# Optimization experiments

Measured on AMD Instinct MI355X. Metric: run time of the kernel, lower is better.

Reference implementation:

```python
import jax, jax.numpy as jnp
import numpy as np

NEG_INF = jnp.finfo(jnp.float32).min


def setup_inputs() -> dict:
    key = jax.random.key(0)
    ks = jax.random.split(key, 5)
    B, S, D = 2, 2048, 1024
    std = 0.02
    return {
        "x": jax.random.normal(ks[0], (B, S, D), dtype=jnp.float32),
        "attention_mask": jnp.ones((B, S), dtype=jnp.int32),
        "Wq": jax.random.normal(ks[1], (D, D), dtype=jnp.float32) * std,
        "Wk": jax.random.normal(ks[2], (D, D), dtype=jnp.float32) * std,
        "Wv": jax.random.normal(ks[3], (D, D), dtype=jnp.float32) * std,
        "Wo": jax.random.normal(ks[4], (D, D), dtype=jnp.float32) * std,
    }


def reference(x, attention_mask, Wq, Wk, Wv, Wo):
    B, S, D = x.shape
    H = 16
    Hd = D // H
    scale = jnp.float32(np.sqrt(Hd))

    # F.linear uses W @ x^T, i.e. x @ W.T
    def proj(x, W):
        return jnp.einsum('bsd,ed->bse', x, W).reshape(B, S, H, Hd).transpose(0, 2, 1, 3)

    q = proj(x, Wq)  # [B,H,S,Hd]
    k = proj(x, Wk)
    v = proj(x, Wv)

    scores = jnp.einsum('bhqd,bhkd->bhqk', q, k) / scale  # [B,H,S,S]
    causal = jnp.triu(jnp.ones((S, S), dtype=bool), k=1)
    scores = jnp.where(causal[None, None, :, :], NEG_INF, scores)
    key_pad = (attention_mask == 0)[:, None, None, :]  # [B,1,1,S]
    scores = jnp.where(key_pad, NEG_INF, scores)

    attn = jax.nn.softmax(scores, axis=-1)
    out = jnp.einsum('bhqk,bhkd->bhqd', attn, v)  # [B,H,S,Hd]
    out = out.transpose(0, 2, 1, 3).reshape(B, S, D)
    return jnp.einsum('bsd,ed->bse', out, Wo)
```

## Files before the change

### kernel.cpp

```cpp
#include <hip/hip_runtime.h>
#include <hip/hip_bf16.h>

typedef __attribute__((ext_vector_type(8))) short bf16x8;
typedef __attribute__((ext_vector_type(4))) short bf16x4;
typedef __attribute__((ext_vector_type(4))) float f32x4;

#define LOG2E 1.4426950408889634f
#define MBIAS 11.541560327111707f
#define NEGF  -3.0e38f

__device__ __forceinline__ void gl_lds16(const void* g, void* l) {
  __builtin_amdgcn_global_load_lds((const __attribute__((address_space(1))) void*)g,
                                   (__attribute__((address_space(3))) void*)l, 16, 0, 0);
}

__device__ __forceinline__ ushort f2bu(float x) {
  __hip_bfloat16 h = __float2bfloat16(x);
  return *(ushort*)&h;
}

__device__ __forceinline__ unsigned int fbits(float x) {
  union { float f; unsigned int u; } c; c.f = x; return c.u;
}

__global__ __launch_bounds__(256) void cast_bf16_k(const float* __restrict__ in,
                                                   ushort* __restrict__ out, int n4) {
  int i = blockIdx.x * 256 + threadIdx.x;
  if (i >= n4) return;
  float4 f = ((const float4*)in)[i];
  ushort4 u;
  u.x = f2bu(f.x); u.y = f2bu(f.y); u.z = f2bu(f.z); u.w = f2bu(f.w);
  ((ushort4*)out)[i] = u;
}

__global__ __launch_bounds__(256) void cast_w4_k(const float* __restrict__ a, const float* __restrict__ b,
                                                 const float* __restrict__ c, const float* __restrict__ d,
                                                 ushort* __restrict__ oa, ushort* __restrict__ ob,
                                                 ushort* __restrict__ oc, ushort* __restrict__ od) {
  int i = blockIdx.x * 256 + threadIdx.x;
  int wsel = i >> 18, j = i & 262143;
  const float* src = wsel == 0 ? a : wsel == 1 ? b : wsel == 2 ? c : d;
  ushort* dst      = wsel == 0 ? oa : wsel == 1 ? ob : wsel == 2 ? oc : od;
  float4 f = ((const float4*)src)[j];
  ushort4 u;
  u.x = f2bu(f.x); u.y = f2bu(f.y); u.z = f2bu(f.z); u.w = f2bu(f.w);
  ((ushort4*)dst)[j] = u;
}

template<int OUT_BF16>
__device__ __forceinline__ void gemm_body(const ushort* __restrict__ A, const ushort* __restrict__ B,
                                          void* __restrict__ C, int M, int N, int Kd, float scale,
                                          int bm, int bn, ushort (*As)[4096], ushort (*Bs)[4096]) {
  const int t  = threadIdx.x;
  const int l  = t & 63;
  const int w  = t >> 6;
  const int lr = l & 15, lg = l >> 4;
  const int wr = (w >> 1) * 64, wc = (w & 1) * 64;

  auto stage = [&](int buf, int ktE) {
    int idx = t, row = idx >> 2, ch = idx & 3;
    gl_lds16(A + (size_t)(bm + row) * Kd + ktE + ch * 8, &As[buf][idx * 8]);
    gl_lds16(B + (size_t)(bn + row) * Kd + ktE + ch * 8, &Bs[buf][idx * 8]);
    idx = t + 256; row = idx >> 2; ch = idx & 3;
    gl_lds16(A + (size_t)(bm + row) * Kd + ktE + ch * 8, &As[buf][idx * 8]);
    gl_lds16(B + (size_t)(bn + row) * Kd + ktE + ch * 8, &Bs[buf][idx * 8]);
  };

  f32x4 acc[4][4] = {};
  const int nK = Kd >> 5;

  stage(0, 0);
  stage(1, 32);
  int cur = 0;
  for (int k5 = 0; k5 < nK; ++k5) {
    if (k5 + 2 < nK) {
      int nb = cur + 2; if (nb >= 3) nb -= 3;
      stage(nb, (k5 + 2) << 5);
      asm volatile("s_waitcnt vmcnt(8)" ::: "memory");
    } else if (k5 + 1 < nK) {
      asm volatile("s_waitcnt vmcnt(4)" ::: "memory");
    } else {
      asm volatile("s_waitcnt vmcnt(0)" ::: "memory");
    }
    __builtin_amdgcn_s_barrier();

    bf16x8 af[4], bfr[4];
#pragma unroll
    for (int m = 0; m < 4; ++m)
      af[m] = *(const bf16x8*)&As[cur][(wr + m * 16 + lr) * 32 + lg * 8];
#pragma unroll
    for (int n = 0; n < 4; ++n)
      bfr[n] = *(const bf16x8*)&Bs[cur][(wc + n * 16 + lr) * 32 + lg * 8];
#pragma unroll
    for (int m = 0; m < 4; ++m)
#pragma unroll
      for (int n = 0; n < 4; ++n)
        acc[m][n] = __builtin_amdgcn_mfma_f32_16x16x32_bf16(af[m], bfr[n], acc[m][n], 0, 0, 0);

    __builtin_amdgcn_s_barrier();
    ++cur; if (cur >= 3) cur -= 3;
  }

#pragma unroll
  for (int m = 0; m < 4; ++m)
#pragma unroll
    for (int n = 0; n < 4; ++n)
#pragma unroll
      for (int j = 0; j < 4; ++j) {
        int row = bm + wr + m * 16 + lg * 4 + j;
        int col = bn + wc + n * 16 + lr;
        float v = acc[m][n][j] * scale;
        if (OUT_BF16) {
          ((ushort*)C)[(size_t)row * N + col] = f2bu(v);
        } else {
          ((float*)C)[(size_t)row * N + col] = v;
        }
      }
}

__global__ __launch_bounds__(256)
void gemm_qkv(const ushort* __restrict__ A, const ushort* __restrict__ Wq, const ushort* __restrict__ Wk,
              const ushort* __restrict__ Wv, ushort* __restrict__ Qo, ushort* __restrict__ Ko,
              ushort* __restrict__ Vo, int M, int Kd) {
  __shared__ __attribute__((aligned(16))) ushort As[3][4096];
  __shared__ __attribute__((aligned(16))) ushort Bs[3][4096];
  int by = blockIdx.y;
  int which = by >> 3;
  const ushort* B = which == 0 ? Wq : which == 1 ? Wk : Wv;
  ushort* C       = which == 0 ? Qo : which == 1 ? Ko : Vo;
  float scale = which == 0 ? 0.125f : 1.0f;
  gemm_body<1>(A, B, C, M, 1024, Kd, scale, blockIdx.x * 128, (by & 7) * 128, As, Bs);
}

__global__ __launch_bounds__(256)
void gemm_out64(const ushort* __restrict__ A, const ushort* __restrict__ B, float* __restrict__ C,
                int M, int N, int Kd) {
  __shared__ __attribute__((aligned(16))) ushort As[3][2048];
  __shared__ __attribute__((aligned(16))) ushort Bs[3][4096];
  const int t  = threadIdx.x;
  const int l  = t & 63;
  const int w  = t >> 6;
  const int lr = l & 15, lg = l >> 4;
  const int wr = (w >> 1) * 32, wc = (w & 1) * 64;
  const int bm = blockIdx.x * 64, bn = blockIdx.y * 128;

  auto stage = [&](int buf, int ktE) {
    int idx = t, row = idx >> 2, ch = idx & 3;
    gl_lds16(A + (size_t)(bm + row) * Kd + ktE + ch * 8, &As[buf][idx * 8]);
    row = idx >> 2; ch = idx & 3;
    gl_lds16(B + (size_t)(bn + row) * Kd + ktE + ch * 8, &Bs[buf][idx * 8]);
    idx = t + 256; row = idx >> 2; ch = idx & 3;
    gl_lds16(B + (size_t)(bn + row) * Kd + ktE + ch * 8, &Bs[buf][idx * 8]);
  };

  f32x4 acc[2][4] = {};
  const int nK = Kd >> 5;

  stage(0, 0);
  stage(1, 32);
  int cur = 0;
  for (int k5 = 0; k5 < nK; ++k5) {
    if (k5 + 2 < nK) {
      int nb = cur + 2; if (nb >= 3) nb -= 3;
      stage(nb, (k5 + 2) << 5);
      asm volatile("s_waitcnt vmcnt(6)" ::: "memory");
    } else if (k5 + 1 < nK) {
      asm volatile("s_waitcnt vmcnt(3)" ::: "memory");
    } else {
      asm volatile("s_waitcnt vmcnt(0)" ::: "memory");
    }
    __builtin_amdgcn_s_barrier();

    bf16x8 af[2], bfr[4];
#pragma unroll
    for (int m = 0; m < 2; ++m)
      af[m] = *(const bf16x8*)&As[cur][(wr + m * 16 + lr) * 32 + lg * 8];
#pragma unroll
    for (int n = 0; n < 4; ++n)
      bfr[n] = *(const bf16x8*)&Bs[cur][(wc + n * 16 + lr) * 32 + lg * 8];
#pragma unroll
    for (int m = 0; m < 2; ++m)
#pragma unroll
      for (int n = 0; n < 4; ++n)
        acc[m][n] = __builtin_amdgcn_mfma_f32_16x16x32_bf16(af[m], bfr[n], acc[m][n], 0, 0, 0);

    __builtin_amdgcn_s_barrier();
    ++cur; if (cur >= 3) cur -= 3;
  }

#pragma unroll
  for (int m = 0; m < 2; ++m)
#pragma unroll
    for (int n = 0; n < 4; ++n)
#pragma unroll
      for (int j = 0; j < 4; ++j) {
        int row = bm + wr + m * 16 + lg * 4 + j;
        int col = bn + wc + n * 16 + lr;
        C[(size_t)row * N + col] = acc[m][n][j];
      }
}

__device__ __forceinline__ void fixed_sm(f32x4 s4[4], float& lacc,
                                         bf16x8& pa0_out, bf16x8& pa1_out) {
#pragma unroll
  for (int c = 0; c < 4; ++c)
#pragma unroll
    for (int j = 0; j < 4; ++j) {
      float p = exp2f(fmaf(s4[c][j], LOG2E, -MBIAS));
      lacc += p;
      s4[c][j] = p;
    }
  union { bf16x8 v; unsigned int w[4]; } pa0, pa1;
#pragma unroll
  for (int c = 0; c < 2; ++c) {
    pa0.w[2 * c + 0] = __builtin_amdgcn_perm(fbits(s4[c][1]), fbits(s4[c][0]), 0x07060302u);
    pa0.w[2 * c + 1] = __builtin_amdgcn_perm(fbits(s4[c][3]), fbits(s4[c][2]), 0x07060302u);
    pa1.w[2 * c + 0] = __builtin_amdgcn_perm(fbits(s4[c + 2][1]), fbits(s4[c + 2][0]), 0x07060302u);
    pa1.w[2 * c + 1] = __builtin_amdgcn_perm(fbits(s4[c + 2][3]), fbits(s4[c + 2][2]), 0x07060302u);
  }
  pa0_out = pa0.v;
  pa1_out = pa1.v;
}

__global__ __launch_bounds__(512, 4)
void attn_k(const ushort* __restrict__ Q, const ushort* __restrict__ K,
            const ushort* __restrict__ V, const int* __restrict__ mask,
            ushort* __restrict__ O) {
  const int S = 2048, D = 1024;
  __shared__ __attribute__((aligned(16))) ushort Ks[4][4096];
  __shared__ __attribute__((aligned(16))) ushort Vs[4][4096];
  __shared__ unsigned long long Msb[32];

  const int t = threadIdx.x;
  const int l = t & 63, w = t >> 6;
  const int lr = l & 15, lg = l >> 4;

  int f = blockIdx.x;
  int pp = (f >> 3) & 15;
  int ss = ((f >> 8) & 1) ? 15 - pp : pp;
  int bh = (f & 7) | (((f >> 7) & 3) << 3);
  int h = bh & 15, b = bh >> 4;
  const int nt = 2 * ss + 2;
  const int np = ss + 1;
  const int q0 = ss * 128;
  const bool hiW = (w >> 2);
  const int npO = hiW ? np : np - 1;
  const int cdi = w & 3;
  const size_t bS = (size_t)b * S;

  const ushort* qptr = Q + (bS + q0 + w * 16 + lr) * D + h * 64;
  bf16x8 qf0 = *(const bf16x8*)(qptr + lg * 8);
  bf16x8 qf1 = *(const bf16x8*)(qptr + 32 + lg * 8);

  const ushort* Kbh = K + bS * D + h * 64;
  const ushort* Vbh = V + bS * D + h * 64;
  const int* mbase = mask + bS;

  int koffA[4], koffB[4];
#pragma unroll
  for (int c = 0; c < 4; ++c) {
    int row = c * 16 + lr;
    koffA[c] = row * 64 + ((lg ^ (row & 7)) << 3);
    koffB[c] = row * 64 + (((4 + lg) ^ (row & 7)) << 3);
  }
  int voff[4];
#pragma unroll
  for (int dt = 0; dt < 4; ++dt) voff[dt] = dt * 1024 + lg * 64 + lr * 4;

  for (int kk = w; kk < nt; kk += 8) {
    unsigned long long mb = __ballot(mbase[kk * 64 + l] != 0);
    if (l == 0) Msb[kk] = mb;
  }
  asm volatile("s_waitcnt lgkmcnt(0)" ::: "memory");
  __builtin_amdgcn_sched_barrier(0);

  float lacc = 0.f;
  f32x4 oE[4] = {}, oO[4] = {};

  auto stage = [&](int p) {
    int s0 = (p & 1) << 1;
    int k0 = 2 * p, k1 = 2 * p + 1;
    { int idx = t; int row = idx >> 3, ch = idx & 7;
      size_t go = (size_t)row * D + ((ch ^ (row & 7)) * 8);
      gl_lds16(Kbh + (size_t)(k0 * 64) * D + go, &Ks[s0][idx * 8]);
      gl_lds16(Kbh + (size_t)(k1 * 64) * D + go, &Ks[s0 + 1][idx * 8]); }
    { int idx = t; int dg = idx >> 7, kq = (idx >> 3) & 15, jj = (idx >> 1) & 3, hf = idx & 1;
      size_t go = (size_t)(kq * 4 + jj) * D + dg * 16 + hf * 8;
      gl_lds16(Vbh + (size_t)(k0 * 64) * D + go, &Vs[s0][idx * 8]);
      gl_lds16(Vbh + (size_t)(k1 * 64) * D + go, &Vs[s0 + 1][idx * 8]); }
  };

  stage(0);
  if (np > 1) stage(1);

  for (int p = 0; p < np; ++p) {
    const int s0 = (p & 1) << 1;
    if (p + 1 < np) asm volatile("s_waitcnt vmcnt(4)" ::: "memory");
    else            asm volatile("s_waitcnt vmcnt(0)" ::: "memory");
    __builtin_amdgcn_s_barrier();

    const bool actO  = (p < npO);
    const bool diagE = (!hiW) && (p == ss);
    const bool diagO = hiW && (p == ss);
    const int cmaxE = diagE ? cdi : 3;
    const int cmaxO = diagO ? cdi : 3;
    unsigned long long mbE = Msb[2 * p];
    unsigned long long mbO = Msb[2 * p + 1];

    f32x4 sE[4], sO[4];
    __builtin_amdgcn_s_setprio(1);
#pragma unroll
    for (int c = 0; c < 4; ++c) {
      if (c <= cmaxE) {
        bf16x8 kf0 = *(const bf16x8*)&Ks[s0][koffA[c]];
        bf16x8 kf1 = *(const bf16x8*)&Ks[s0][koffB[c]];
        f32x4 sc = {0.f, 0.f, 0.f, 0.f};
        sc = __builtin_amdgcn_mfma_f32_16x16x32_bf16(kf0, qf0, sc, 0, 0, 0);
        sc = __builtin_amdgcn_mfma_f32_16x16x32_bf16(kf1, qf1, sc, 0, 0, 0);
        if (diagE && c == cmaxE) {
          int qg = cdi * 16 + lr, kb = c * 16 + lg * 4;
#pragma unroll
          for (int j = 0; j < 4; ++j)
            if (kb + j > qg) sc[j] = NEGF;
        }
        sE[c] = sc;
      } else {
        sE[c] = (f32x4){NEGF, NEGF, NEGF, NEGF};
      }
      if (actO) {
        if (c <= cmaxO) {
          bf16x8 kf0 = *(const bf16x8*)&Ks[s0 + 1][koffA[c]];
          bf16x8 kf1 = *(const bf16x8*)&Ks[s0 + 1][koffB[c]];
          f32x4 sc = {0.f, 0.f, 0.f, 0.f};
          sc = __builtin_amdgcn_mfma_f32_16x16x32_bf16(kf0, qf0, sc, 0, 0, 0);
          sc = __builtin_amdgcn_mfma_f32_16x16x32_bf16(kf1, qf1, sc, 0, 0, 0);
          if (diagO && c == cmaxO) {
            int qg = cdi * 16 + lr, kb = c * 16 + lg * 4;
#pragma unroll
            for (int j = 0; j < 4; ++j)
              if (kb + j > qg) sc[j] = NEGF;
          }
          sO[c] = sc;
        } else {
          sO[c] = (f32x4){NEGF, NEGF, NEGF, NEGF};
        }
      }
    }
    __builtin_amdgcn_s_setprio(0);

    if (~mbE != 0ull) {
#pragma unroll
      for (int c = 0; c < 4; ++c)
#pragma unroll
        for (int j = 0; j < 4; ++j)
          if (!((mbE >> (c * 16 + lg * 4 + j)) & 1)) sE[c][j] = NEGF;
    }
    if (actO && (~mbO != 0ull)) {
#pragma unroll
      for (int c = 0; c < 4; ++c)
#pragma unroll
        for (int j = 0; j < 4; ++j)
          if (!((mbO >> (c * 16 + lg * 4 + j)) & 1)) sO[c][j] = NEGF;
    }

    bf16x8 paE0, paE1;
    fixed_sm(sE, lacc, paE0, paE1);
    __builtin_amdgcn_s_setprio(1);
#pragma unroll
    for (int dt = 0; dt < 4; ++dt) {
      const __attribute__((address_space(3))) ushort* vp =
          (const __attribute__((address_space(3))) ushort*)&Vs[s0][0] + voff[dt];
      bf16x4 h0, h1, h2, h3;
      asm volatile(
          "ds_read_b64_tr_b16 %0, %4\n\t"
          "ds_read_b64_tr_b16 %1, %4 offset:512\n\t"
          "ds_read_b64_tr_b16 %2, %4 offset:1024\n\t"
          "ds_read_b64_tr_b16 %3, %4 offset:1536\n\t"
          "s_waitcnt lgkmcnt(0)"
          : "=&v"(h0), "=&v"(h1), "=&v"(h2), "=&v"(h3)
          : "v"(vp));
      bf16x8 vb0 = __builtin_shufflevector(h0, h1, 0, 1, 2, 3, 4, 5, 6, 7);
      bf16x8 vb1 = __builtin_shufflevector(h2, h3, 0, 1, 2, 3, 4, 5, 6, 7);
      oE[dt] = __builtin_amdgcn_mfma_f32_16x16x32_bf16(paE0, vb0, oE[dt], 0, 0, 0);
      oE[dt] = __builtin_amdgcn_mfma_f32_16x16x32_bf16(paE1, vb1, oE[dt], 0, 0, 0);
    }
    __builtin_amdgcn_s_setprio(0);

    if (actO) {
      bf16x8 paO0, paO1;
      fixed_sm(sO, lacc, paO0, paO1);
      __builtin_amdgcn_s_setprio(1);
#pragma unroll
      for (int dt = 0; dt < 4; ++dt) {
        const __attribute__((address_space(3))) ushort* vp =
            (const __attribute__((address_space(3))) ushort*)&Vs[s0 + 1][0] + voff[dt];
        bf16x4 h0, h1, h2, h3;
        asm volatile(
            "ds_read_b64_tr_b16 %0, %4\n\t"
            "ds_read_b64_tr_b16 %1, %4 offset:512\n\t"
            "ds_read_b64_tr_b16 %2, %4 offset:1024\n\t"
            "ds_read_b64_tr_b16 %3, %4 offset:1536\n\t"
            "s_waitcnt lgkmcnt(0)"
            : "=&v"(h0), "=&v"(h1), "=&v"(h2), "=&v"(h3)
            : "v"(vp));
        bf16x8 vb0 = __builtin_shufflevector(h0, h1, 0, 1, 2, 3, 4, 5, 6, 7);
        bf16x8 vb1 = __builtin_shufflevector(h2, h3, 0, 1, 2, 3, 4, 5, 6, 7);
        oO[dt] = __builtin_amdgcn_mfma_f32_16x16x32_bf16(paO0, vb0, oO[dt], 0, 0, 0);
        oO[dt] = __builtin_amdgcn_mfma_f32_16x16x32_bf16(paO1, vb1, oO[dt], 0, 0, 0);
      }
      __builtin_amdgcn_s_setprio(0);
    }

    __builtin_amdgcn_s_barrier();
    if (p + 2 < np) stage(p + 2);
  }

  lacc += __shfl_xor(lacc, 16);
  lacc += __shfl_xor(lacc, 32);
  float inv = 1.0f / lacc;
  float v0 = __shfl(inv, lg * 4 + 0, 16);
  float v1 = __shfl(inv, lg * 4 + 1, 16);
  float v2 = __shfl(inv, lg * 4 + 2, 16);
  float v3 = __shfl(inv, lg * 4 + 3, 16);
#pragma unroll
  for (int dt = 0; dt < 4; ++dt) {
    size_t col = (size_t)h * 64 + dt * 16 + lr;
    size_t r0 = bS + q0 + w * 16 + lg * 4;
    O[(r0 + 0) * D + col] = f2bu((oE[dt][0] + oO[dt][0]) * v0);
    O[(r0 + 1) * D + col] = f2bu((oE[dt][1] + oO[dt][1]) * v1);
    O[(r0 + 2) * D + col] = f2bu((oE[dt][2] + oO[dt][2]) * v2);
    O[(r0 + 3) * D + col] = f2bu((oE[dt][3] + oO[dt][3]) * v3);
  }
}

extern "C" void kernel_launch(void* const* d_in, const int* in_sizes, int n_in,
                              void* d_out, int out_size, void* d_ws, size_t ws_size,
                              hipStream_t stream) {
  const float* x    = (const float*)d_in[0];
  const int*   mask = (const int*)d_in[1];
  const float* Wq   = (const float*)d_in[2];
  const float* Wk   = (const float*)d_in[3];
  const float* Wv   = (const float*)d_in[4];
  const float* Wo   = (const float*)d_in[5];
  float* out = (float*)d_out;

  const int B = 2, S = 2048, D = 1024;
  const int M = B * S;

  char* ws = (char*)d_ws;
  ushort* xb  = (ushort*)(ws);
  ushort* wqb = (ushort*)(ws + (8ull  << 20));
  ushort* wkb = (ushort*)(ws + (10ull << 20));
  ushort* wvb = (ushort*)(ws + (12ull << 20));
  ushort* wob = (ushort*)(ws + (14ull << 20));
  ushort* Qb  = (ushort*)(ws + (16ull << 20));
  ushort* Kb  = (ushort*)(ws + (24ull << 20));
  ushort* Vb  = (ushort*)(ws + (32ull << 20));
  ushort* AO  = (ushort*)(ws + (40ull << 20));

  int nx4 = M * D / 4;
  cast_bf16_k<<<(nx4 + 255) / 256, 256, 0, stream>>>(x, xb, nx4);
  cast_w4_k<<<4096, 256, 0, stream>>>(Wq, Wk, Wv, Wo, wqb, wkb, wvb, wob);

  dim3 gq(M / 128, 24);
  gemm_qkv<<<gq, 256, 0, stream>>>(xb, wqb, wkb, wvb, Qb, Kb, Vb, M, D);

  attn_k<<<512, 512, 0, stream>>>(Qb, Kb, Vb, mask, AO);

  dim3 go(M / 64, D / 128);
  gemm_out64<<<go, 256, 0, stream>>>(AO, wob, out, M, D, D);
}
```

Measured before the change: 113.7 us.

## Merge cast kernels, compute softmax row sums via MFMA, drop setprio

Folds the activation and weight bf16 casts into one launch, which removes one kernel launch and its tail. The per-lane softmax denominator accumulation and the cross-lane shuffles are replaced by MFMA products of the bf16 probabilities with a ones vector, so each row sum lands directly in the output layout. This offloads VALU adds to the matrix unit but sums the bf16-rounded probabilities, which now match the values multiplied into V. The s_setprio priority hints around the MFMA sections are also removed.

```diff
diff --git a/kernel.cpp b/kernel.cpp
--- a/kernel.cpp
+++ b/kernel.cpp
@@ -23,24 +23,21 @@
   union { float f; unsigned int u; } c; c.f = x; return c.u;
 }
 
-__global__ __launch_bounds__(256) void cast_bf16_k(const float* __restrict__ in,
-                                                   ushort* __restrict__ out, int n4) {
+__global__ __launch_bounds__(256)
+void cast_all_k(const float* __restrict__ x, const float* __restrict__ a, const float* __restrict__ b,
+                const float* __restrict__ c, const float* __restrict__ d,
+                ushort* __restrict__ ox, ushort* __restrict__ oa, ushort* __restrict__ ob,
+                ushort* __restrict__ oc, ushort* __restrict__ od) {
   int i = blockIdx.x * 256 + threadIdx.x;
-  if (i >= n4) return;
-  float4 f = ((const float4*)in)[i];
-  ushort4 u;
-  u.x = f2bu(f.x); u.y = f2bu(f.y); u.z = f2bu(f.z); u.w = f2bu(f.w);
-  ((ushort4*)out)[i] = u;
-}
-
-__global__ __launch_bounds__(256) void cast_w4_k(const float* __restrict__ a, const float* __restrict__ b,
-                                                 const float* __restrict__ c, const float* __restrict__ d,
-                                                 ushort* __restrict__ oa, ushort* __restrict__ ob,
-                                                 ushort* __restrict__ oc, ushort* __restrict__ od) {
-  int i = blockIdx.x * 256 + threadIdx.x;
-  int wsel = i >> 18, j = i & 262143;
-  const float* src = wsel == 0 ? a : wsel == 1 ? b : wsel == 2 ? c : d;
-  ushort* dst      = wsel == 0 ? oa : wsel == 1 ? ob : wsel == 2 ? oc : od;
+  const float* src; ushort* dst; int j;
+  if (i < 1048576) {
+    src = x; dst = ox; j = i;
+  } else {
+    int k = i - 1048576;
+    int wsel = k >> 18; j = k & 262143;
+    src = wsel == 0 ? a : wsel == 1 ? b : wsel == 2 ? c : d;
+    dst = wsel == 0 ? oa : wsel == 1 ? ob : wsel == 2 ? oc : od;
+  }
   float4 f = ((const float4*)src)[j];
   ushort4 u;
   u.x = f2bu(f.x); u.y = f2bu(f.y); u.z = f2bu(f.z); u.w = f2bu(f.w);
@@ -200,16 +197,12 @@
       }
 }
 
-__device__ __forceinline__ void fixed_sm(f32x4 s4[4], float& lacc,
-                                         bf16x8& pa0_out, bf16x8& pa1_out) {
+__device__ __forceinline__ void fixed_sm(f32x4 s4[4], bf16x8& pa0_out, bf16x8& pa1_out) {
 #pragma unroll
   for (int c = 0; c < 4; ++c)
 #pragma unroll
-    for (int j = 0; j < 4; ++j) {
-      float p = exp2f(fmaf(s4[c][j], LOG2E, -MBIAS));
-      lacc += p;
-      s4[c][j] = p;
-    }
+    for (int j = 0; j < 4; ++j)
+      s4[c][j] = exp2f(fmaf(s4[c][j], LOG2E, -MBIAS));
   union { bf16x8 v; unsigned int w[4]; } pa0, pa1;
 #pragma unroll
   for (int c = 0; c < 2; ++c) {
@@ -256,6 +249,10 @@
   const ushort* Vbh = V + bS * D + h * 64;
   const int* mbase = mask + bS;
 
+  bf16x8 onesf;
+#pragma unroll
+  for (int i = 0; i < 8; ++i) onesf[i] = (short)0x3F80;
+
   int koffA[4], koffB[4];
 #pragma unroll
   for (int c = 0; c < 4; ++c) {
@@ -274,7 +271,7 @@
   asm volatile("s_waitcnt lgkmcnt(0)" ::: "memory");
   __builtin_amdgcn_sched_barrier(0);
 
-  float lacc = 0.f;
+  f32x4 lsum = {0.f, 0.f, 0.f, 0.f};
   f32x4 oE[4] = {}, oO[4] = {};
 
   auto stage = [&](int p) {
@@ -308,7 +305,6 @@
     unsigned long long mbO = Msb[2 * p + 1];
 
     f32x4 sE[4], sO[4];
-    __builtin_amdgcn_s_setprio(1);
 #pragma unroll
     for (int c = 0; c < 4; ++c) {
       if (c <= cmaxE) {
@@ -346,7 +342,6 @@
         }
       }
     }
-    __builtin_amdgcn_s_setprio(0);
 
     if (~mbE != 0ull) {
 #pragma unroll
@@ -364,8 +359,9 @@
     }
 
     bf16x8 paE0, paE1;
-    fixed_sm(sE, lacc, paE0, paE1);
-    __builtin_amdgcn_s_setprio(1);
+    fixed_sm(sE, paE0, paE1);
+    lsum = __builtin_amdgcn_mfma_f32_16x16x32_bf16(paE0, onesf, lsum, 0, 0, 0);
+    lsum = __builtin_amdgcn_mfma_f32_16x16x32_bf16(paE1, onesf, lsum, 0, 0, 0);
 #pragma unroll
     for (int dt = 0; dt < 4; ++dt) {
       const __attribute__((address_space(3))) ushort* vp =
@@ -384,12 +380,12 @@
       oE[dt] = __builtin_amdgcn_mfma_f32_16x16x32_bf16(paE0, vb0, oE[dt], 0, 0, 0);
       oE[dt] = __builtin_amdgcn_mfma_f32_16x16x32_bf16(paE1, vb1, oE[dt], 0, 0, 0);
     }
-    __builtin_amdgcn_s_setprio(0);
 
     if (actO) {
       bf16x8 paO0, paO1;
-      fixed_sm(sO, lacc, paO0, paO1);
-      __builtin_amdgcn_s_setprio(1);
+      fixed_sm(sO, paO0, paO1);
+      lsum = __builtin_amdgcn_mfma_f32_16x16x32_bf16(paO0, onesf, lsum, 0, 0, 0);
+      lsum = __builtin_amdgcn_mfma_f32_16x16x32_bf16(paO1, onesf, lsum, 0, 0, 0);
 #pragma unroll
       for (int dt = 0; dt < 4; ++dt) {
         const __attribute__((address_space(3))) ushort* vp =
@@ -408,28 +404,24 @@
         oO[dt] = __builtin_amdgcn_mfma_f32_16x16x32_bf16(paO0, vb0, oO[dt], 0, 0, 0);
         oO[dt] = __builtin_amdgcn_mfma_f32_16x16x32_bf16(paO1, vb1, oO[dt], 0, 0, 0);
       }
-      __builtin_amdgcn_s_setprio(0);
     }
 
     __builtin_amdgcn_s_barrier();
     if (p + 2 < np) stage(p + 2);
   }
 
-  lacc += __shfl_xor(lacc, 16);
-  lacc += __shfl_xor(lacc, 32);
-  float inv = 1.0f / lacc;
-  float v0 = __shfl(inv, lg * 4 + 0, 16);
-  float v1 = __shfl(inv, lg * 4 + 1, 16);
-  float v2 = __shfl(inv, lg * 4 + 2, 16);
-  float v3 = __shfl(inv, lg * 4 + 3, 16);
+  float iv0 = 1.0f / lsum[0];
+  float iv1 = 1.0f / lsum[1];
+  float iv2 = 1.0f / lsum[2];
+  float iv3 = 1.0f / lsum[3];
 #pragma unroll
   for (int dt = 0; dt < 4; ++dt) {
     size_t col = (size_t)h * 64 + dt * 16 + lr;
     size_t r0 = bS + q0 + w * 16 + lg * 4;
-    O[(r0 + 0) * D + col] = f2bu((oE[dt][0] + oO[dt][0]) * v0);
-    O[(r0 + 1) * D + col] = f2bu((oE[dt][1] + oO[dt][1]) * v1);
-    O[(r0 + 2) * D + col] = f2bu((oE[dt][2] + oO[dt][2]) * v2);
-    O[(r0 + 3) * D + col] = f2bu((oE[dt][3] + oO[dt][3]) * v3);
+    O[(r0 + 0) * D + col] = f2bu((oE[dt][0] + oO[dt][0]) * iv0);
+    O[(r0 + 1) * D + col] = f2bu((oE[dt][1] + oO[dt][1]) * iv1);
+    O[(r0 + 2) * D + col] = f2bu((oE[dt][2] + oO[dt][2]) * iv2);
+    O[(r0 + 3) * D + col] = f2bu((oE[dt][3] + oO[dt][3]) * iv3);
   }
 }
 
@@ -458,9 +450,7 @@
   ushort* Vb  = (ushort*)(ws + (32ull << 20));
   ushort* AO  = (ushort*)(ws + (40ull << 20));
 
-  int nx4 = M * D / 4;
-  cast_bf16_k<<<(nx4 + 255) / 256, 256, 0, stream>>>(x, xb, nx4);
-  cast_w4_k<<<4096, 256, 0, stream>>>(Wq, Wk, Wv, Wo, wqb, wkb, wvb, wob);
+  cast_all_k<<<8192, 256, 0, stream>>>(x, Wq, Wk, Wv, Wo, xb, wqb, wkb, wvb, wob);
 
   dim3 gq(M / 128, 24);
   gemm_qkv<<<gq, 256, 0, stream>>>(xb, wqb, wkb, wvb, Qb, Kb, Vb, M, D);
```

After: 112.1 us. About the same (-1.4%).
